# Performance work log

Measured on AMD Instinct MI355X. Metric: run time of the kernel, lower is better.

The kernel has to match this reference:

```python
import jax, jax.numpy as jnp
import numpy as np

DIM = 768
HEADS = 12
HEAD_DIM = DIM // HEADS  # 64
GRID = 48               # H = W = 48 tokens
RANK = 8                # LoRA rank


def setup_inputs() -> dict:
    key = jax.random.key(0)
    ks = jax.random.split(key, 20)
    s = 0.02
    inp = {
        "x": jax.random.normal(ks[0], (1, GRID, GRID, DIM), dtype=jnp.float32),
        "Wq": jax.random.normal(ks[1], (DIM, DIM), dtype=jnp.float32) * s,
        "bq": jax.random.normal(ks[2], (DIM,), dtype=jnp.float32) * s,
        "Wk": jax.random.normal(ks[3], (DIM, DIM), dtype=jnp.float32) * s,
        "bk": jax.random.normal(ks[4], (DIM,), dtype=jnp.float32) * s,
        "Wv": jax.random.normal(ks[5], (DIM, DIM), dtype=jnp.float32) * s,
        "bv": jax.random.normal(ks[6], (DIM,), dtype=jnp.float32) * s,
        "Wp": jax.random.normal(ks[7], (DIM, DIM), dtype=jnp.float32) * s,
        "bp": jax.random.normal(ks[8], (DIM,), dtype=jnp.float32) * s,
        "rel_pos_h": jax.random.normal(ks[9], (2 * GRID - 1, HEAD_DIM), dtype=jnp.float32) * s,
        "rel_pos_w": jax.random.normal(ks[10], (2 * GRID - 1, HEAD_DIM), dtype=jnp.float32) * s,
        "Aq": jax.random.normal(ks[11], (DIM, RANK), dtype=jnp.float32) * s,
        "Bq": jax.random.normal(ks[12], (RANK, DIM), dtype=jnp.float32) * s,
        "Ak": jax.random.normal(ks[13], (DIM, RANK), dtype=jnp.float32) * s,
        "Bk": jax.random.normal(ks[14], (RANK, DIM), dtype=jnp.float32) * s,
        "Av": jax.random.normal(ks[15], (DIM, RANK), dtype=jnp.float32) * s,
        "Bv": jax.random.normal(ks[16], (RANK, DIM), dtype=jnp.float32) * s,
    }
    return inp


def _get_rel_pos(size, rel_pos):
    # q_size == k_size == size, rel_pos has exactly 2*size-1 rows -> direct lookup
    idx = jnp.arange(size)[:, None] - jnp.arange(size)[None, :] + (size - 1)
    return rel_pos[idx]  # (size, size, head_dim)


def reference(x, Wq, bq, Wk, bk, Wv, bv, Wp, bp, rel_pos_h, rel_pos_w,
              Aq, Bq, Ak, Bk, Av, Bv):
    B, H, W, _ = x.shape
    N = H * W
    scale = HEAD_DIM ** -0.5

    # QKV projections + LoRA additions
    q = x @ Wq + bq + (x @ Aq) @ Bq
    k = x @ Wk + bk + (x @ Ak) @ Bk
    v = x @ Wv + bv + (x @ Av) @ Bv

    # (B, heads, N, head_dim)
    q = q.reshape(B, N, HEADS, HEAD_DIM).transpose(0, 2, 1, 3)
    k = k.reshape(B, N, HEADS, HEAD_DIM).transpose(0, 2, 1, 3)
    v = v.reshape(B, N, HEADS, HEAD_DIM).transpose(0, 2, 1, 3)

    attn = jnp.einsum('bhnc,bhmc->bhnm', q, k) * scale  # (B, heads, N, N)

    # Decomposed relative position bias (SAM add_decomposed_rel_pos)
    Rh = _get_rel_pos(H, rel_pos_h)  # (H, H, c)
    Rw = _get_rel_pos(W, rel_pos_w)  # (W, W, c)
    r_q = q.reshape(B, HEADS, H, W, HEAD_DIM)
    rel_h = jnp.einsum('bnhwc,hkc->bnhwk', r_q, Rh)  # (B, heads, H, W, H)
    rel_w = jnp.einsum('bnhwc,wkc->bnhwk', r_q, Rw)  # (B, heads, H, W, W)
    attn = (attn.reshape(B, HEADS, H, W, H, W)
            + rel_h[..., :, None] + rel_w[..., None, :]).reshape(B, HEADS, N, N)

    attn = jax.nn.softmax(attn, axis=-1)
    out = jnp.einsum('bhnm,bhmc->bhnc', attn, v)        # (B, heads, N, c)
    out = out.transpose(0, 2, 1, 3).reshape(B, H, W, DIM)
    return out @ Wp + bp
```

## Files before the change

kernel.cpp:

```cpp
#include <hip/hip_runtime.h>


#define DIM   768
#define HEADS 12
#define HD    64
#define NTOK  2304
#define RANK  8
#define GRD   48
#define CHUNKS 4
#define LOG2E 1.44269504088896f

typedef __attribute__((ext_vector_type(8))) short bf16x8;
typedef __attribute__((ext_vector_type(4))) float f32x4;
typedef unsigned short ushort_t;

__device__ __forceinline__ unsigned short f2bf(float x) {
    union { float f; unsigned u; } v; v.f = x;
    unsigned r = v.u + 0x7fffu + ((v.u >> 16) & 1u);
    return (unsigned short)(r >> 16);
}
__device__ __forceinline__ float bf2f(unsigned short h) {
    return __uint_as_float(((unsigned)h) << 16);
}
__device__ __forceinline__ void gload_lds16(const ushort_t* g, ushort_t* l) {
    __builtin_amdgcn_global_load_lds(
        (const __attribute__((address_space(1))) unsigned int*)g,
        (__attribute__((address_space(3))) unsigned int*)l, 16, 0, 0);
}

__global__ __launch_bounds__(256) void k_prep(
    const float* __restrict__ x, ushort_t* __restrict__ xb,
    const float* __restrict__ rph, const float* __restrict__ rpw,
    ushort_t* __restrict__ rphb, ushort_t* __restrict__ rpwb,
    const float* __restrict__ Wq, const float* __restrict__ Wk,
    const float* __restrict__ Wv, const float* __restrict__ Wp,
    const float* __restrict__ Aq, const float* __restrict__ Bq,
    const float* __restrict__ Ak, const float* __restrict__ Bk,
    const float* __restrict__ Av, const float* __restrict__ Bv,
    ushort_t* __restrict__ WT) {
    int bid = blockIdx.x, tid = threadIdx.x;

    if (bid < 1740) {
        if (bid < 1728) {
            int idx = (bid * 256 + tid) * 4;
            float4 v = *(const float4*)(x + idx);
            ushort4 o = make_ushort4(f2bf(v.x), f2bf(v.y), f2bf(v.z), f2bf(v.w));
            *(ushort4*)(xb + idx) = o;
        } else {
            int e = ((bid - 1728) * 256 + tid) * 4;
            const int TSZ = (2 * GRD - 1) * HD;
            if (e < TSZ) {
                float4 v = *(const float4*)(rph + e);
                ushort4 o = make_ushort4(f2bf(v.x), f2bf(v.y), f2bf(v.z), f2bf(v.w));
                *(ushort4*)(rphb + e) = o;
            } else if (e < 2 * TSZ) {
                float4 v = *(const float4*)(rpw + e - TSZ);
                ushort4 o = make_ushort4(f2bf(v.x), f2bf(v.y), f2bf(v.z), f2bf(v.w));
                *(ushort4*)(rpwb + e - TSZ) = o;
            }
        }
    }

    int kb = (bid % 24) * 32;
    int nb = (bid / 24) * 32;
    int sel = nb / DIM, nmod = nb % DIM;
    const float* W = (sel == 0) ? Wq : (sel == 1) ? Wk : (sel == 2) ? Wv : Wp;
    const float* A = (sel == 0) ? Aq : (sel == 1) ? Ak : Av;
    const float* B = (sel == 0) ? Bq : (sel == 1) ? Bk : Bv;
    __shared__ float T[32][33];
    for (int i = tid; i < 1024; i += 256) {
        int kl = i >> 5, nl = i & 31;
        float v = W[(kb + kl) * DIM + nmod + nl];
        if (sel < 3) {
            #pragma unroll
            for (int r = 0; r < RANK; r++)
                v += A[(kb + kl) * RANK + r] * B[r * DIM + nmod + nl];
        }
        T[kl][nl] = v;
    }
    __syncthreads();
    for (int i = tid; i < 1024; i += 256) {
        int nl = i >> 5, kl = i & 31;
        WT[(size_t)(nb + nl) * DIM + kb + kl] = f2bf(T[kl][nl]);
    }
}

__global__ __launch_bounds__(256) void k_gemm_qkv(
    const ushort_t* __restrict__ xb, const ushort_t* __restrict__ WT,
    const float* __restrict__ bq, const float* __restrict__ bk,
    const float* __restrict__ bv,
    ushort_t* __restrict__ Qb, ushort_t* __restrict__ Kb,
    ushort_t* __restrict__ Vtb) {
    __shared__ __align__(16) ushort_t As[128 * 32];
    __shared__ __align__(16) ushort_t Bs[64 * 32];
    int tid = threadIdx.x;
    int wave = tid >> 6, lane = tid & 63, quad = lane >> 4, l16 = lane & 15;
    int wx = wave & 1, wy = wave >> 1;
    int nb = blockIdx.x * 64, mb = blockIdx.y * 128;

    f32x4 zero = {0.f, 0.f, 0.f, 0.f};
    f32x4 acc[4][2];
    #pragma unroll
    for (int i = 0; i < 4; i++)
        #pragma unroll
        for (int j = 0; j < 2; j++) acc[i][j] = zero;

    int rl = lane >> 2;
    int cl = (lane & 3) * 8;
    const ushort_t* gA = xb + (size_t)(mb + wave * 32 + rl) * DIM + cl;
    const ushort_t* gB = WT + (size_t)(nb + wave * 16 + rl) * DIM + cl;
    ushort_t* lA = &As[(wave * 32) * 32];
    ushort_t* lB = &Bs[(wave * 16) * 32];

    for (int k0 = 0; k0 < DIM; k0 += 32) {
        __syncthreads();
        gload_lds16(gA + k0,            lA);
        gload_lds16(gA + k0 + 16 * DIM, lA + 16 * 32);
        gload_lds16(gB + k0,            lB);
        __syncthreads();
        bf16x8 af[4], bf[2];
        #pragma unroll
        for (int i = 0; i < 4; i++)
            af[i] = *(const bf16x8*)&As[(wy * 64 + i * 16 + l16) * 32 + quad * 8];
        #pragma unroll
        for (int j = 0; j < 2; j++)
            bf[j] = *(const bf16x8*)&Bs[(wx * 32 + j * 16 + l16) * 32 + quad * 8];
        #pragma unroll
        for (int i = 0; i < 4; i++)
            #pragma unroll
            for (int j = 0; j < 2; j++)
                acc[i][j] = __builtin_amdgcn_mfma_f32_16x16x32_bf16(af[i], bf[j], acc[i][j], 0, 0, 0);
    }

    #pragma unroll
    for (int j = 0; j < 2; j++) {
        int col = nb + wx * 32 + j * 16 + l16;
        int sel = col / DIM, rem = col % DIM;
        int hh = rem >> 6, cc = rem & 63;
        const float* bias = (sel == 0) ? bq : (sel == 1) ? bk : bv;
        float bval = bias[rem];
        #pragma unroll
        for (int i = 0; i < 4; i++) {
            #pragma unroll
            for (int r = 0; r < 4; r++) {
                int row = mb + wy * 64 + i * 16 + quad * 4 + r;
                unsigned short o = f2bf(acc[i][j][r] + bval);
                if (sel == 0)      Qb[(size_t)(hh * NTOK + row) * HD + cc] = o;
                else if (sel == 1) Kb[(size_t)(hh * NTOK + row) * HD + cc] = o;
                else               Vtb[(size_t)(hh * HD + cc) * NTOK + row] = o;
            }
        }
    }
}

__global__ __launch_bounds__(256) void k_relmm(
    const ushort_t* __restrict__ Qb, const ushort_t* __restrict__ rphb,
    const ushort_t* __restrict__ rpwb, float* __restrict__ relH,
    float* __restrict__ relW) {
    int id = blockIdx.x * 4 + (threadIdx.x >> 6);
    int lane = threadIdx.x & 63, quad = lane >> 4, l16 = lane & 15;
    bool isW = id >= 576;
    int t = isW ? id - 576 : id;
    int h = t / GRD, g = t % GRD;
    const ushort_t* tab = isW ? rpwb : rphb;
    float* outp = isW ? relW : relH;

    f32x4 zero = {0.f, 0.f, 0.f, 0.f};
    f32x4 acc[3][3];
    #pragma unroll
    for (int i = 0; i < 3; i++)
        #pragma unroll
        for (int j = 0; j < 3; j++) acc[i][j] = zero;

    bf16x8 bfr[3][2];
    #pragma unroll
    for (int ct = 0; ct < 3; ct++) {
        int trow = g + 47 - (ct * 16 + l16);
        bfr[ct][0] = *(const bf16x8*)&tab[(size_t)trow * HD + quad * 8];
        bfr[ct][1] = *(const bf16x8*)&tab[(size_t)trow * HD + 32 + quad * 8];
    }
    #pragma unroll
    for (int ms = 0; ms < 3; ms++) {
        int m = ms * 16 + l16;
        int n = isW ? m * GRD + g : g * GRD + m;
        bf16x8 a0 = *(const bf16x8*)&Qb[(size_t)(h * NTOK + n) * HD + quad * 8];
        bf16x8 a1 = *(const bf16x8*)&Qb[(size_t)(h * NTOK + n) * HD + 32 + quad * 8];
        #pragma unroll
        for (int ct = 0; ct < 3; ct++) {
            acc[ms][ct] = __builtin_amdgcn_mfma_f32_16x16x32_bf16(a0, bfr[ct][0], acc[ms][ct], 0, 0, 0);
            acc[ms][ct] = __builtin_amdgcn_mfma_f32_16x16x32_bf16(a1, bfr[ct][1], acc[ms][ct], 0, 0, 0);
        }
    }
    #pragma unroll
    for (int ms = 0; ms < 3; ms++) {
        #pragma unroll
        for (int ct = 0; ct < 3; ct++) {
            #pragma unroll
            for (int r = 0; r < 4; r++) {
                int m = ms * 16 + quad * 4 + r;
                int n = isW ? m * GRD + g : g * GRD + m;
                int col = ct * 16 + l16;
                outp[(size_t)(h * NTOK + n) * GRD + col] = acc[ms][ct][r] * LOG2E;
            }
        }
    }
}

__global__ __launch_bounds__(256) void k_attn(
    const ushort_t* __restrict__ Qb, const ushort_t* __restrict__ Kb,
    const ushort_t* __restrict__ Vtb, const float* __restrict__ relH,
    const float* __restrict__ relW, float* __restrict__ Opart,
    float* __restrict__ Lpart) {
    int h = blockIdx.x >> 2, chunk = blockIdx.x & 3, qt = blockIdx.y;
    int tid = threadIdx.x;
    int wave = tid >> 6, lane = tid & 63, quad = lane >> 4, l16 = lane & 15;
    int qbase = qt * 128;
    int kbase = chunk * 576;

    __shared__ __align__(16) ushort_t Ks[64 * 68];
    __shared__ __align__(16) ushort_t Vs[64 * 68];
    __shared__ __align__(16) ushort_t Ps[4][32 * 68];
    __shared__ __align__(16) ushort_t rws[128 * 52];
    __shared__ __align__(16) ushort_t rhs[128 * 14];

    for (int i = tid; i < 128 * 48; i += 256) {
        int r = i / 48, c = i % 48;
        rws[r * 52 + c] = f2bf(relW[(size_t)(h * NTOK + qbase + r) * GRD + c]);
    }
    for (int i = tid; i < 128 * 12; i += 256) {
        int r = i / 12, c = i % 12;
        rhs[r * 14 + c] = f2bf(relH[(size_t)(h * NTOK + qbase + r) * GRD + chunk * 12 + c]);
    }

    bf16x8 qf[2][2];
    #pragma unroll
    for (int s = 0; s < 2; s++) {
        int qrow = qbase + wave * 32 + s * 16 + l16;
        qf[s][0] = *(const bf16x8*)&Qb[(size_t)(h * NTOK + qrow) * HD + quad * 8];
        qf[s][1] = *(const bf16x8*)&Qb[(size_t)(h * NTOK + qrow) * HD + 32 + quad * 8];
    }

    int r0 = tid >> 3, c0 = (tid & 7) * 8;
    const ushort_t* kg0 = Kb + (size_t)(h * NTOK + r0) * HD + c0;
    const ushort_t* kg1 = Kb + (size_t)(h * NTOK + r0 + 32) * HD + c0;
    const ushort_t* vg0 = Vtb + (size_t)(h * HD + r0) * NTOK + c0;
    const ushort_t* vg1 = Vtb + (size_t)(h * HD + r0 + 32) * NTOK + c0;
    int sk0 = r0 * 68 + c0, sk1 = sk0 + 32 * 68;

    float lacc[2] = {0.f, 0.f};
    f32x4 zero = {0.f, 0.f, 0.f, 0.f};
    f32x4 oacc[2][4];
    #pragma unroll
    for (int s = 0; s < 2; s++)
        #pragma unroll
        for (int cs = 0; cs < 4; cs++) oacc[s][cs] = zero;

    const float scale2 = 0.125f * LOG2E;

    uint4 rk0 = *(const uint4*)(kg0 + (size_t)kbase * HD);
    uint4 rk1 = *(const uint4*)(kg1 + (size_t)kbase * HD);
    uint4 rv0 = *(const uint4*)(vg0 + kbase);
    uint4 rv1 = *(const uint4*)(vg1 + kbase);

    for (int kt = 0; kt < 9; kt++) {
        int kb = kbase + kt * 64;
        __syncthreads();
        *(uint4*)&Ks[sk0] = rk0;  *(uint4*)&Ks[sk1] = rk1;
        *(uint4*)&Vs[sk0] = rv0;  *(uint4*)&Vs[sk1] = rv1;
        __syncthreads();
        if (kt < 8) {
            int kbn = kb + 64;
            rk0 = *(const uint4*)(kg0 + (size_t)kbn * HD);
            rk1 = *(const uint4*)(kg1 + (size_t)kbn * HD);
            rv0 = *(const uint4*)(vg0 + kbn);
            rv1 = *(const uint4*)(vg1 + kbn);
        }

        #pragma unroll
        for (int ks = 0; ks < 4; ks++) {
            bf16x8 kf0 = *(const bf16x8*)&Ks[(ks * 16 + l16) * 68 + quad * 8];
            bf16x8 kf1 = *(const bf16x8*)&Ks[(ks * 16 + l16) * 68 + 32 + quad * 8];
            f32x4 st[2];
            #pragma unroll
            for (int s = 0; s < 2; s++) {
                f32x4 z = zero;
                z = __builtin_amdgcn_mfma_f32_16x16x32_bf16(kf0, qf[s][0], z, 0, 0, 0);
                z = __builtin_amdgcn_mfma_f32_16x16x32_bf16(kf1, qf[s][1], z, 0, 0, 0);
                st[s] = z;
            }
            int kb4 = kb + ks * 16 + quad * 4;
            int kh = kb4 / 48;
            int khl = kh - chunk * 12;
            int kw0 = kb4 - kh * 48;
            #pragma unroll
            for (int s = 0; s < 2; s++) {
                int row = wave * 32 + s * 16 + l16;
                float rh = bf2f(rhs[row * 14 + khl]);
                uint2 u = *(const uint2*)&rws[row * 52 + kw0];
                float p0 = __builtin_amdgcn_exp2f(st[s][0] * scale2 + rh + __uint_as_float(u.x << 16));
                float p1 = __builtin_amdgcn_exp2f(st[s][1] * scale2 + rh + __uint_as_float(u.x & 0xffff0000u));
                float p2 = __builtin_amdgcn_exp2f(st[s][2] * scale2 + rh + __uint_as_float(u.y << 16));
                float p3 = __builtin_amdgcn_exp2f(st[s][3] * scale2 + rh + __uint_as_float(u.y & 0xffff0000u));
                lacc[s] += (p0 + p1) + (p2 + p3);
                uint2 w;
                w.x = __builtin_amdgcn_perm(__float_as_uint(p1), __float_as_uint(p0), 0x07060302u);
                w.y = __builtin_amdgcn_perm(__float_as_uint(p3), __float_as_uint(p2), 0x07060302u);
                *(uint2*)&Ps[wave][(s * 16 + l16) * 68 + ks * 16 + quad * 4] = w;
            }
        }

        bf16x8 vf[4][2];
        #pragma unroll
        for (int cs = 0; cs < 4; cs++) {
            vf[cs][0] = *(const bf16x8*)&Vs[(cs * 16 + l16) * 68 + quad * 8];
            vf[cs][1] = *(const bf16x8*)&Vs[(cs * 16 + l16) * 68 + 32 + quad * 8];
        }
        #pragma unroll
        for (int s = 0; s < 2; s++) {
            bf16x8 pa0 = *(const bf16x8*)&Ps[wave][(s * 16 + l16) * 68 + quad * 8];
            bf16x8 pa1 = *(const bf16x8*)&Ps[wave][(s * 16 + l16) * 68 + 32 + quad * 8];
            #pragma unroll
            for (int cs = 0; cs < 4; cs++) {
                oacc[s][cs] = __builtin_amdgcn_mfma_f32_16x16x32_bf16(pa0, vf[cs][0], oacc[s][cs], 0, 0, 0);
                oacc[s][cs] = __builtin_amdgcn_mfma_f32_16x16x32_bf16(pa1, vf[cs][1], oacc[s][cs], 0, 0, 0);
            }
        }
    }

    #pragma unroll
    for (int s = 0; s < 2; s++) {
        float l = lacc[s];
        l += __shfl_xor(l, 16);
        l += __shfl_xor(l, 32);
        lacc[s] = l;
    }

    size_t obase = (size_t)(chunk * HEADS + h) * NTOK;
    #pragma unroll
    for (int s = 0; s < 2; s++) {
        #pragma unroll
        for (int cs = 0; cs < 4; cs++) {
            #pragma unroll
            for (int r = 0; r < 4; r++) {
                int row = qbase + wave * 32 + s * 16 + quad * 4 + r;
                Opart[(obase + row) * HD + cs * 16 + l16] = oacc[s][cs][r];
            }
        }
        if (quad == 0)
            Lpart[obase + qbase + wave * 32 + s * 16 + l16] = lacc[s];
    }
}

__global__ __launch_bounds__(256) void k_merge(const float* __restrict__ Opart,
                                               const float* __restrict__ Lpart,
                                               ushort_t* __restrict__ Ob) {
    int t = blockIdx.x * 256 + threadIdx.x;
    int e = t * 4;
    int c = e & (HD - 1);
    int row = (e >> 6) % NTOK;
    int h = e / (NTOK * HD);
    const int ostride = HEADS * NTOK * HD;
    float4 s = {0.f, 0.f, 0.f, 0.f};
    float l = 0.f;
    #pragma unroll
    for (int ch = 0; ch < CHUNKS; ch++) {
        float4 v = *(const float4*)&Opart[(size_t)ch * ostride + e];
        s.x += v.x; s.y += v.y; s.z += v.z; s.w += v.w;
        l += Lpart[(size_t)(ch * HEADS + h) * NTOK + row];
    }
    float inv = 1.0f / l;
    ushort4 o = make_ushort4(f2bf(s.x * inv), f2bf(s.y * inv),
                             f2bf(s.z * inv), f2bf(s.w * inv));
    *(ushort4*)&Ob[(size_t)row * DIM + h * HD + c] = o;
}

__global__ __launch_bounds__(256) void k_gemm_proj(
    const ushort_t* __restrict__ Ob, const ushort_t* __restrict__ WTp,
    const float* __restrict__ bp, float* __restrict__ out) {
    __shared__ __align__(16) ushort_t As[128 * 32];
    __shared__ __align__(16) ushort_t Bs[64 * 32];
    int tid = threadIdx.x;
    int wave = tid >> 6, lane = tid & 63, quad = lane >> 4, l16 = lane & 15;
    int wx = wave & 1, wy = wave >> 1;
    int nb = blockIdx.x * 64, mb = blockIdx.y * 128;

    f32x4 zero = {0.f, 0.f, 0.f, 0.f};
    f32x4 acc[4][2];
    #pragma unroll
    for (int i = 0; i < 4; i++)
        #pragma unroll
        for (int j = 0; j < 2; j++) acc[i][j] = zero;

    int rl = lane >> 2;
    int cl = (lane & 3) * 8;
    const ushort_t* gA = Ob + (size_t)(mb + wave * 32 + rl) * DIM + cl;
    const ushort_t* gB = WTp + (size_t)(nb + wave * 16 + rl) * DIM + cl;
    ushort_t* lA = &As[(wave * 32) * 32];
    ushort_t* lB = &Bs[(wave * 16) * 32];

    for (int k0 = 0; k0 < DIM; k0 += 32) {
        __syncthreads();
        gload_lds16(gA + k0,            lA);
        gload_lds16(gA + k0 + 16 * DIM, lA + 16 * 32);
        gload_lds16(gB + k0,            lB);
        __syncthreads();
        bf16x8 af[4], bf[2];
        #pragma unroll
        for (int i = 0; i < 4; i++)
            af[i] = *(const bf16x8*)&As[(wy * 64 + i * 16 + l16) * 32 + quad * 8];
        #pragma unroll
        for (int j = 0; j < 2; j++)
            bf[j] = *(const bf16x8*)&Bs[(wx * 32 + j * 16 + l16) * 32 + quad * 8];
        #pragma unroll
        for (int i = 0; i < 4; i++)
            #pragma unroll
            for (int j = 0; j < 2; j++)
                acc[i][j] = __builtin_amdgcn_mfma_f32_16x16x32_bf16(af[i], bf[j], acc[i][j], 0, 0, 0);
    }

    #pragma unroll
    for (int j = 0; j < 2; j++) {
        int col = nb + wx * 32 + j * 16 + l16;
        float bval = bp[col];
        #pragma unroll
        for (int i = 0; i < 4; i++) {
            #pragma unroll
            for (int r = 0; r < 4; r++) {
                int row = mb + wy * 64 + i * 16 + quad * 4 + r;
                out[(size_t)row * DIM + col] = acc[i][j][r] + bval;
            }
        }
    }
}

extern "C" void kernel_launch(void* const* d_in, const int* in_sizes, int n_in,
                              void* d_out, int out_size, void* d_ws, size_t ws_size,
                              hipStream_t stream) {
    const float* x   = (const float*)d_in[0];
    const float* Wq  = (const float*)d_in[1];
    const float* bq  = (const float*)d_in[2];
    const float* Wk  = (const float*)d_in[3];
    const float* bk  = (const float*)d_in[4];
    const float* Wv  = (const float*)d_in[5];
    const float* bv  = (const float*)d_in[6];
    const float* Wp  = (const float*)d_in[7];
    const float* bp  = (const float*)d_in[8];
    const float* rph = (const float*)d_in[9];
    const float* rpw = (const float*)d_in[10];
    const float* Aq  = (const float*)d_in[11];
    const float* Bq  = (const float*)d_in[12];
    const float* Ak  = (const float*)d_in[13];
    const float* Bk  = (const float*)d_in[14];
    const float* Av  = (const float*)d_in[15];
    const float* Bv  = (const float*)d_in[16];
    float* out = (float*)d_out;

    char* w = (char*)d_ws;
    size_t off = 0;
    auto carve = [&](size_t bytes) {
        char* p = w + off;
        off += (bytes + 255) & ~(size_t)255;
        return p;
    };
    ushort_t* xb    = (ushort_t*)carve((size_t)NTOK * DIM * 2);
    ushort_t* WT    = (ushort_t*)carve((size_t)4 * DIM * DIM * 2);
    ushort_t* Qb    = (ushort_t*)carve((size_t)HEADS * NTOK * HD * 2);
    ushort_t* Kb    = (ushort_t*)carve((size_t)HEADS * NTOK * HD * 2);
    ushort_t* Vtb   = (ushort_t*)carve((size_t)HEADS * HD * NTOK * 2);
    float*    relH  = (float*)carve((size_t)HEADS * NTOK * GRD * 4);
    float*    relW  = (float*)carve((size_t)HEADS * NTOK * GRD * 4);
    ushort_t* Ob    = (ushort_t*)carve((size_t)NTOK * DIM * 2);
    float*    Opart = (float*)carve((size_t)CHUNKS * HEADS * NTOK * HD * 4);
    float*    Lpart = (float*)carve((size_t)CHUNKS * HEADS * NTOK * 4);
    ushort_t* rphb  = (ushort_t*)carve((size_t)(2 * GRD - 1) * HD * 2);
    ushort_t* rpwb  = (ushort_t*)carve((size_t)(2 * GRD - 1) * HD * 2);

    k_prep<<<dim3(2304), dim3(256), 0, stream>>>(
        x, xb, rph, rpw, rphb, rpwb,
        Wq, Wk, Wv, Wp, Aq, Bq, Ak, Bk, Av, Bv, WT);
    k_gemm_qkv<<<dim3(36, 18), dim3(256), 0, stream>>>(
        xb, WT, bq, bk, bv, Qb, Kb, Vtb);
    k_relmm<<<dim3(288), dim3(256), 0, stream>>>(
        Qb, rphb, rpwb, relH, relW);
    k_attn<<<dim3(HEADS * CHUNKS, NTOK / 128), dim3(256), 0, stream>>>(
        Qb, Kb, Vtb, relH, relW, Opart, Lpart);
    k_merge<<<dim3(HEADS * NTOK * HD / (256 * 4)), dim3(256), 0, stream>>>(
        Opart, Lpart, Ob);
    k_gemm_proj<<<dim3(12, 18), dim3(256), 0, stream>>>(
        Ob, WT + (size_t)3 * DIM * DIM, bp, out);
}
```

Measured before the change: 200.9 us.

## Pass P through registers via lane shuffles and fuse split-K merge into projection GEMM

In the attention kernel, the softmax probabilities no longer make a round trip through the per-wave LDS buffer Ps. They are rearranged into MFMA A-operand layout with cross-lane shuffles, processing keys in two 32-column halves, which also cuts LDS use. Separately, the k_merge kernel and the bf16 Ob buffer are removed. The projection GEMM now sums the four fp32 Opart chunks, normalises by the summed Lpart, and converts to bf16 while staging its A tile. This saves a launch and an intermediate write and read, at the cost of each N-tile block re-reading the fp32 partials (12 column blocks each read them).

```diff
diff --git a/kernel.cpp b/kernel.cpp
--- a/kernel.cpp
+++ b/kernel.cpp
@@ -9,6 +9,7 @@
 #define GRD   48
 #define CHUNKS 4
 #define LOG2E 1.44269504088896f
+#define OSTR  (HEADS * NTOK * HD)
 
 typedef __attribute__((ext_vector_type(8))) short bf16x8;
 typedef __attribute__((ext_vector_type(4))) float f32x4;
@@ -26,6 +27,12 @@
     __builtin_amdgcn_global_load_lds(
         (const __attribute__((address_space(1))) unsigned int*)g,
         (__attribute__((address_space(3))) unsigned int*)l, 16, 0, 0);
+}
+__device__ __forceinline__ bf16x8 mk_bf16x8(unsigned a, unsigned b,
+                                            unsigned c, unsigned d) {
+    union { unsigned u[4]; bf16x8 v; } t;
+    t.u[0] = a; t.u[1] = b; t.u[2] = c; t.u[3] = d;
+    return t.v;
 }
 
 __global__ __launch_bounds__(256) void k_prep(
@@ -219,7 +226,6 @@
 
     __shared__ __align__(16) ushort_t Ks[64 * 68];
     __shared__ __align__(16) ushort_t Vs[64 * 68];
-    __shared__ __align__(16) ushort_t Ps[4][32 * 68];
     __shared__ __align__(16) ushort_t rws[128 * 52];
     __shared__ __align__(16) ushort_t rhs[128 * 14];
 
@@ -256,6 +262,8 @@
         for (int cs = 0; cs < 4; cs++) oacc[s][cs] = zero;
 
     const float scale2 = 0.125f * LOG2E;
+    int src0 = l16 + ((quad & 1) << 5);
+    int src1 = src0 + 16;
 
     uint4 rk0 = *(const uint4*)(kg0 + (size_t)kbase * HD);
     uint4 rk1 = *(const uint4*)(kg1 + (size_t)kbase * HD);
@@ -277,53 +285,65 @@
         }
 
         #pragma unroll
-        for (int ks = 0; ks < 4; ks++) {
-            bf16x8 kf0 = *(const bf16x8*)&Ks[(ks * 16 + l16) * 68 + quad * 8];
-            bf16x8 kf1 = *(const bf16x8*)&Ks[(ks * 16 + l16) * 68 + 32 + quad * 8];
-            f32x4 st[2];
+        for (int half = 0; half < 2; half++) {
+            uint2 w[2][2];
+            #pragma unroll
+            for (int ks = 0; ks < 2; ks++) {
+                int kcol = half * 32 + ks * 16;
+                bf16x8 kf0 = *(const bf16x8*)&Ks[(kcol + l16) * 68 + quad * 8];
+                bf16x8 kf1 = *(const bf16x8*)&Ks[(kcol + l16) * 68 + 32 + quad * 8];
+                f32x4 st[2];
+                #pragma unroll
+                for (int s = 0; s < 2; s++) {
+                    f32x4 z = zero;
+                    z = __builtin_amdgcn_mfma_f32_16x16x32_bf16(kf0, qf[s][0], z, 0, 0, 0);
+                    z = __builtin_amdgcn_mfma_f32_16x16x32_bf16(kf1, qf[s][1], z, 0, 0, 0);
+                    st[s] = z;
+                }
+                int kb4 = kb + kcol + quad * 4;
+                int kh = kb4 / 48;
+                int khl = kh - chunk * 12;
+                int kw0 = kb4 - kh * 48;
+                #pragma unroll
+                for (int s = 0; s < 2; s++) {
+                    int row = wave * 32 + s * 16 + l16;
+                    float rh = bf2f(rhs[row * 14 + khl]);
+                    uint2 u = *(const uint2*)&rws[row * 52 + kw0];
+                    float p0 = __builtin_amdgcn_exp2f(st[s][0] * scale2 + rh + __uint_as_float(u.x << 16));
+                    float p1 = __builtin_amdgcn_exp2f(st[s][1] * scale2 + rh + __uint_as_float(u.x & 0xffff0000u));
+                    float p2 = __builtin_amdgcn_exp2f(st[s][2] * scale2 + rh + __uint_as_float(u.y << 16));
+                    float p3 = __builtin_amdgcn_exp2f(st[s][3] * scale2 + rh + __uint_as_float(u.y & 0xffff0000u));
+                    lacc[s] += (p0 + p1) + (p2 + p3);
+                    w[s][ks].x = __builtin_amdgcn_perm(__float_as_uint(p1), __float_as_uint(p0), 0x07060302u);
+                    w[s][ks].y = __builtin_amdgcn_perm(__float_as_uint(p3), __float_as_uint(p2), 0x07060302u);
+                }
+            }
+
+            bf16x8 pa[2];
             #pragma unroll
             for (int s = 0; s < 2; s++) {
-                f32x4 z = zero;
-                z = __builtin_amdgcn_mfma_f32_16x16x32_bf16(kf0, qf[s][0], z, 0, 0, 0);
-                z = __builtin_amdgcn_mfma_f32_16x16x32_bf16(kf1, qf[s][1], z, 0, 0, 0);
-                st[s] = z;
-            }
-            int kb4 = kb + ks * 16 + quad * 4;
-            int kh = kb4 / 48;
-            int khl = kh - chunk * 12;
-            int kw0 = kb4 - kh * 48;
-            #pragma unroll
-            for (int s = 0; s < 2; s++) {
-                int row = wave * 32 + s * 16 + l16;
-                float rh = bf2f(rhs[row * 14 + khl]);
-                uint2 u = *(const uint2*)&rws[row * 52 + kw0];
-                float p0 = __builtin_amdgcn_exp2f(st[s][0] * scale2 + rh + __uint_as_float(u.x << 16));
-                float p1 = __builtin_amdgcn_exp2f(st[s][1] * scale2 + rh + __uint_as_float(u.x & 0xffff0000u));
-                float p2 = __builtin_amdgcn_exp2f(st[s][2] * scale2 + rh + __uint_as_float(u.y << 16));
-                float p3 = __builtin_amdgcn_exp2f(st[s][3] * scale2 + rh + __uint_as_float(u.y & 0xffff0000u));
-                lacc[s] += (p0 + p1) + (p2 + p3);
-                uint2 w;
-                w.x = __builtin_amdgcn_perm(__float_as_uint(p1), __float_as_uint(p0), 0x07060302u);
-                w.y = __builtin_amdgcn_perm(__float_as_uint(p3), __float_as_uint(p2), 0x07060302u);
-                *(uint2*)&Ps[wave][(s * 16 + l16) * 68 + ks * 16 + quad * 4] = w;
-            }
-        }
-
-        bf16x8 vf[4][2];
-        #pragma unroll
-        for (int cs = 0; cs < 4; cs++) {
-            vf[cs][0] = *(const bf16x8*)&Vs[(cs * 16 + l16) * 68 + quad * 8];
-            vf[cs][1] = *(const bf16x8*)&Vs[(cs * 16 + l16) * 68 + 32 + quad * 8];
-        }
-        #pragma unroll
-        for (int s = 0; s < 2; s++) {
-            bf16x8 pa0 = *(const bf16x8*)&Ps[wave][(s * 16 + l16) * 68 + quad * 8];
-            bf16x8 pa1 = *(const bf16x8*)&Ps[wave][(s * 16 + l16) * 68 + 32 + quad * 8];
-            #pragma unroll
-            for (int cs = 0; cs < 4; cs++) {
-                oacc[s][cs] = __builtin_amdgcn_mfma_f32_16x16x32_bf16(pa0, vf[cs][0], oacc[s][cs], 0, 0, 0);
-                oacc[s][cs] = __builtin_amdgcn_mfma_f32_16x16x32_bf16(pa1, vf[cs][1], oacc[s][cs], 0, 0, 0);
-            }
+                unsigned a0 = (unsigned)__shfl((int)w[s][0].x, src0);
+                unsigned a1 = (unsigned)__shfl((int)w[s][0].y, src0);
+                unsigned a2 = (unsigned)__shfl((int)w[s][0].x, src1);
+                unsigned a3 = (unsigned)__shfl((int)w[s][0].y, src1);
+                unsigned b0 = (unsigned)__shfl((int)w[s][1].x, src0);
+                unsigned b1 = (unsigned)__shfl((int)w[s][1].y, src0);
+                unsigned b2 = (unsigned)__shfl((int)w[s][1].x, src1);
+                unsigned b3 = (unsigned)__shfl((int)w[s][1].y, src1);
+                bool lo = (quad < 2);
+                pa[s] = mk_bf16x8(lo ? a0 : b0, lo ? a1 : b1,
+                                  lo ? a2 : b2, lo ? a3 : b3);
+            }
+
+            bf16x8 vf[4];
+            #pragma unroll
+            for (int cs = 0; cs < 4; cs++)
+                vf[cs] = *(const bf16x8*)&Vs[(cs * 16 + l16) * 68 + half * 32 + quad * 8];
+            #pragma unroll
+            for (int s = 0; s < 2; s++)
+                #pragma unroll
+                for (int cs = 0; cs < 4; cs++)
+                    oacc[s][cs] = __builtin_amdgcn_mfma_f32_16x16x32_bf16(pa[s], vf[cs], oacc[s][cs], 0, 0, 0);
         }
     }
 
@@ -351,38 +371,26 @@
     }
 }
 
-__global__ __launch_bounds__(256) void k_merge(const float* __restrict__ Opart,
-                                               const float* __restrict__ Lpart,
-                                               ushort_t* __restrict__ Ob) {
-    int t = blockIdx.x * 256 + threadIdx.x;
-    int e = t * 4;
-    int c = e & (HD - 1);
-    int row = (e >> 6) % NTOK;
-    int h = e / (NTOK * HD);
-    const int ostride = HEADS * NTOK * HD;
-    float4 s = {0.f, 0.f, 0.f, 0.f};
-    float l = 0.f;
-    #pragma unroll
-    for (int ch = 0; ch < CHUNKS; ch++) {
-        float4 v = *(const float4*)&Opart[(size_t)ch * ostride + e];
-        s.x += v.x; s.y += v.y; s.z += v.z; s.w += v.w;
-        l += Lpart[(size_t)(ch * HEADS + h) * NTOK + row];
-    }
-    float inv = 1.0f / l;
-    ushort4 o = make_ushort4(f2bf(s.x * inv), f2bf(s.y * inv),
-                             f2bf(s.z * inv), f2bf(s.w * inv));
-    *(ushort4*)&Ob[(size_t)row * DIM + h * HD + c] = o;
-}
-
 __global__ __launch_bounds__(256) void k_gemm_proj(
-    const ushort_t* __restrict__ Ob, const ushort_t* __restrict__ WTp,
-    const float* __restrict__ bp, float* __restrict__ out) {
+    const float* __restrict__ Opart, const float* __restrict__ Lpart,
+    const ushort_t* __restrict__ WTp, const float* __restrict__ bp,
+    float* __restrict__ out) {
     __shared__ __align__(16) ushort_t As[128 * 32];
     __shared__ __align__(16) ushort_t Bs[64 * 32];
+    __shared__ float Ls[12 * 128];
     int tid = threadIdx.x;
     int wave = tid >> 6, lane = tid & 63, quad = lane >> 4, l16 = lane & 15;
     int wx = wave & 1, wy = wave >> 1;
-    int nb = blockIdx.x * 64, mb = blockIdx.y * 128;
+    int mb = blockIdx.x * 128, nb = blockIdx.y * 64;
+
+    for (int e = tid; e < 12 * 128; e += 256) {
+        int hh = e >> 7, r = e & 127;
+        float l = 0.f;
+        #pragma unroll
+        for (int ch = 0; ch < CHUNKS; ch++)
+            l += Lpart[(size_t)(ch * HEADS + hh) * NTOK + mb + r];
+        Ls[e] = 1.0f / l;
+    }
 
     f32x4 zero = {0.f, 0.f, 0.f, 0.f};
     f32x4 acc[4][2];
@@ -391,18 +399,37 @@
         #pragma unroll
         for (int j = 0; j < 2; j++) acc[i][j] = zero;
 
-    int rl = lane >> 2;
-    int cl = (lane & 3) * 8;
-    const ushort_t* gA = Ob + (size_t)(mb + wave * 32 + rl) * DIM + cl;
+    int rl = lane >> 2, cl = (lane & 3) * 8;
     const ushort_t* gB = WTp + (size_t)(nb + wave * 16 + rl) * DIM + cl;
-    ushort_t* lA = &As[(wave * 32) * 32];
     ushort_t* lB = &Bs[(wave * 16) * 32];
 
+    int r2 = tid >> 1, chalf = (tid & 1) * 16;
+
     for (int k0 = 0; k0 < DIM; k0 += 32) {
+        int h0 = k0 >> 6;
+        int cb = (k0 & 63) + chalf;
         __syncthreads();
-        gload_lds16(gA + k0,            lA);
-        gload_lds16(gA + k0 + 16 * DIM, lA + 16 * 32);
-        gload_lds16(gB + k0,            lB);
+        gload_lds16(gB + k0, lB);
+        float linv = Ls[h0 * 128 + r2];
+        size_t abase = ((size_t)h0 * NTOK + mb + r2) * HD + cb;
+        float4 sA[4];
+        #pragma unroll
+        for (int i = 0; i < 4; i++) sA[i] = make_float4(0.f, 0.f, 0.f, 0.f);
+        #pragma unroll
+        for (int ch = 0; ch < CHUNKS; ch++) {
+            const float* p = Opart + (size_t)ch * OSTR + abase;
+            #pragma unroll
+            for (int i = 0; i < 4; i++) {
+                float4 v = *(const float4*)(p + i * 4);
+                sA[i].x += v.x; sA[i].y += v.y; sA[i].z += v.z; sA[i].w += v.w;
+            }
+        }
+        #pragma unroll
+        for (int i = 0; i < 4; i++) {
+            ushort4 o = make_ushort4(f2bf(sA[i].x * linv), f2bf(sA[i].y * linv),
+                                     f2bf(sA[i].z * linv), f2bf(sA[i].w * linv));
+            *(ushort4*)&As[r2 * 32 + chalf + i * 4] = o;
+        }
         __syncthreads();
         bf16x8 af[4], bf[2];
         #pragma unroll
@@ -469,7 +496,6 @@
     ushort_t* Vtb   = (ushort_t*)carve((size_t)HEADS * HD * NTOK * 2);
     float*    relH  = (float*)carve((size_t)HEADS * NTOK * GRD * 4);
     float*    relW  = (float*)carve((size_t)HEADS * NTOK * GRD * 4);
-    ushort_t* Ob    = (ushort_t*)carve((size_t)NTOK * DIM * 2);
     float*    Opart = (float*)carve((size_t)CHUNKS * HEADS * NTOK * HD * 4);
     float*    Lpart = (float*)carve((size_t)CHUNKS * HEADS * NTOK * 4);
     ushort_t* rphb  = (ushort_t*)carve((size_t)(2 * GRD - 1) * HD * 2);
@@ -484,8 +510,6 @@
         Qb, rphb, rpwb, relH, relW);
     k_attn<<<dim3(HEADS * CHUNKS, NTOK / 128), dim3(256), 0, stream>>>(
         Qb, Kb, Vtb, relH, relW, Opart, Lpart);
-    k_merge<<<dim3(HEADS * NTOK * HD / (256 * 4)), dim3(256), 0, stream>>>(
-        Opart, Lpart, Ob);
-    k_gemm_proj<<<dim3(12, 18), dim3(256), 0, stream>>>(
-        Ob, WT + (size_t)3 * DIM * DIM, bp, out);
-}
+    k_gemm_proj<<<dim3(18, 12), dim3(256), 0, stream>>>(
+        Opart, Lpart, WT + (size_t)3 * DIM * DIM, bp, out);
+}
```

Result: slower. 227.3 us (+13.2%).
